# Optimization experiments

Hardware: AMD Instinct MI355X
Metric: run time of the kernel (lower is better)

The kernel has to match this reference:

```python
import jax, jax.numpy as jnp
import numpy as np

B, T, Fd, C, D = 16, 256, 128, 32, 32
K_RATIO = 0.5
EPS = 1e-5


def setup_inputs() -> dict:
    key = jax.random.key(0)
    ks = jax.random.split(key, 40)
    n = lambda i, shape, s=0.05: jax.random.normal(ks[i], shape, jnp.float32) * s
    inp = {"x": jax.random.normal(ks[0], (B, T, Fd, C), jnp.float32)}
    inp.update(c1w=n(1, (C, C)), c1b=n(2, (C,)), bng=1.0 + n(3, (C,)), bnb=n(4, (C,)),
               bnm=n(5, (C,)), bnv=jax.random.uniform(ks[6], (C,)) + 0.5,
               c2w=n(7, (1, C)), c2b=n(8, (1,)))
    def gat_params(i0, pre):
        return {pre + "apw": n(i0, (D, C)), pre + "apb": n(i0 + 1, (D,)),
                pre + "aw": n(i0 + 2, (D,)), pre + "pww": n(i0 + 3, (D, C)),
                pre + "pwb": n(i0 + 4, (D,)), pre + "pow": n(i0 + 5, (D, C)),
                pre + "pob": n(i0 + 6, (D,)), pre + "g": 1.0 + n(i0 + 7, (D,)),
                pre + "be": n(i0 + 8, (D,)), pre + "m": n(i0 + 9, (D,)),
                pre + "v": jax.random.uniform(ks[i0 + 10], (D,)) + 0.5}
    inp.update(gat_params(9, "fc_"))
    inp.update(gat_params(20, "tc_"))
    inp.update(pfw=n(31, (1, D)), pfb=n(32, (1,)), ptw=n(33, (1, D)), ptb=n(34, (1,)),
               w1=n(35, (D, D)), w2=n(36, (D, D)), fcw=n(37, (2, 2 * D)), fcb=n(38, (2,)))
    return inp


def _gat(h, apw, apb, aw, pww, pwb, poww, pob, g, be, mu, var):
    # h: (B, N, C). Dense pairwise multiplication -> (B, N, N, C)
    p = h[:, :, None, :] * h[:, None, :, :]
    e = jnp.tanh(jnp.einsum('bijc,dc->bijd', p, apw) + apb)      # (B,N,N,D)
    att = jax.nn.softmax(jnp.einsum('bijd,d->bij', e, aw), axis=2)  # softmax over dim=-2 (temp=1)
    out = jnp.einsum('bij,bjc->bic', att, h) @ pww.T + pwb + h @ poww.T + pob
    out = (out - mu) / jnp.sqrt(var + EPS) * g + be               # BatchNorm1d (eval)
    return jax.nn.selu(out)


def _pool(h, pw, pb, ratio):
    s = jax.nn.sigmoid(h @ pw.T + pb)                # (B,N,1)
    kn = max(int(h.shape[1] * ratio), 1)
    _, idx = jax.lax.top_k(s[..., 0], kn)            # (B,kn), descending scores
    return jnp.take_along_axis(h * s, idx[..., None], axis=1)


def reference(x, c1w, c1b, bng, bnb, bnm, bnv, c2w, c2b,
              fc_apw, fc_apb, fc_aw, fc_pww, fc_pwb, fc_pow, fc_pob, fc_g, fc_be, fc_m, fc_v,
              tc_apw, tc_apb, tc_aw, tc_pww, tc_pwb, tc_pow, tc_pob, tc_g, tc_be, tc_m, tc_v,
              pfw, pfb, ptw, ptb, w1, w2, fcw, fcb):
    # conv1 (1x1), SELU, BatchNorm2d (eval), conv2 (1x1 -> 1 channel)
    xp = jnp.einsum('oc,btfc->botf', c1w, x) + c1b[None, :, None, None]
    xp = jax.nn.selu(xp)
    xp = (xp - bnm[None, :, None, None]) / jnp.sqrt(bnv + EPS)[None, :, None, None] \
         * bng[None, :, None, None] + bnb[None, :, None, None]
    m = jnp.einsum('c,bctf->btf', c2w[0], xp) + c2b[0]           # (B,T,F)
    M0 = jax.nn.softmax(m, axis=1)
    FCatt = jnp.einsum('btf,btfc->bfc', M0, x)                   # sum over T
    TCatt = jnp.einsum('btf,btfc->btc', M0, x)                   # sum over F
    FC_gat = _gat(FCatt, fc_apw, fc_apb, fc_aw, fc_pww, fc_pwb, fc_pow, fc_pob, fc_g, fc_be, fc_m, fc_v)
    TC_gat = _gat(TCatt, tc_apw, tc_apb, tc_aw, tc_pww, tc_pwb, tc_pow, tc_pob, tc_g, tc_be, tc_m, tc_v)
    xF = _pool(FC_gat, pfw, pfb, K_RATIO)                        # (B, F/2, D)
    xT = _pool(TC_gat, ptw, ptb, K_RATIO)                        # (B, T/2, D)
    M1 = jax.nn.softmax((xF @ w1.T) @ xT.transpose(0, 2, 1), axis=-1)
    M2 = jax.nn.softmax((xT @ w2.T) @ xF.transpose(0, 2, 1), axis=-1)
    xF_fused = xF + M1 @ xT
    xT_fused = xT + M2 @ xF
    node = jnp.concatenate([xF_fused.max(axis=1), xT_fused.max(axis=1)], axis=-1)
    return node @ fcw.T + fcb
```

## Files before the change

kernel.cpp:

```cpp
#include <hip/hip_runtime.h>
#include <hip/hip_bf16.h>

#define Bn 16
#define Tn 256
#define Fn 128
#define Cn 32
#define Dn 32
#define EPSf 1e-5f
#define SELU_L 1.0507009873554805f
#define SELU_A 1.6732632423543772f

typedef unsigned short u16;
typedef unsigned int u32;
typedef __attribute__((ext_vector_type(8))) short bf16x8;
typedef __attribute__((ext_vector_type(4))) float f32x4;

struct Ptrs { const void* p[39]; };

#define P_C1W 0
#define P_C1B 1024
#define P_MW  1056
#define P_MK  1088
#define P_FC  1089
#define P_TCG (1089+3264)
#define G_APW 0
#define G_APB 1024
#define G_AW  1056
#define G_PWW 1088
#define G_PWB 2112
#define G_POW 2144
#define G_POB 3168
#define G_GS  3200
#define G_GB  3232
#define GAT_SZ 3264
#define P_PFW (P_TCG+GAT_SZ)
#define P_PFB (P_PFW+32)
#define P_PTW (P_PFB+1)
#define P_PTB (P_PTW+32)
#define P_W1  (P_PTB+1)
#define P_W2  (P_W1+1024)
#define P_FCW (P_W2+1024)
#define P_FCB (P_FCW+128)
#define P_FLAG 10000

#define WS_M     10240
#define WS_FCATT (WS_M+524288)
#define WS_TCATT (WS_FCATT+65536)
#define WS_FCGAT (WS_TCATT+131072)
#define WS_TCGAT (WS_FCGAT+65536)
#define WS_XF    (WS_TCGAT+131072)
#define WS_XT    (WS_XF+32768)
#define WS_XFF   (WS_XT+65536)
#define WS_XTF   (WS_XFF+32768)

__device__ __forceinline__ float bf2f(u16 u) {
    union { u32 i; float f; } v; v.i = ((u32)u) << 16; return v.f;
}
__device__ __forceinline__ u16 f2bf(float f) {
    union { float f; u32 u; } v; v.f = f;
    u32 r = (v.u + 0x7fffu + ((v.u >> 16) & 1u)) >> 16;
    return (u16)r;
}
__device__ __forceinline__ u32 cvt_pk_bf16(float lo, float hi) {
    u32 r;
    asm("v_cvt_pk_bf16_f32 %0, %1, %2" : "=v"(r) : "v"(lo), "v"(hi));
    return r;
}
__device__ __forceinline__ void up2(u32 u, float* o) {
    union { u32 i; float f; } a, b;
    a.i = u << 16; b.i = u & 0xffff0000u;
    o[0] = a.f; o[1] = b.f;
}
__device__ __forceinline__ float tanh_fast(float x) {
    float e = __expf(2.f * x);
    return 1.f - 2.f / (e + 1.f);
}
__device__ __forceinline__ float ldp(const void* p, int i, int isb) {
    return isb ? bf2f(((const u16*)p)[i]) : ((const float*)p)[i];
}

__global__ __launch_bounds__(256) void k0_setup(Ptrs in, float* __restrict__ P) {
    __shared__ int sflag;
    int tid = threadIdx.x;
    int blk = blockIdx.x;
    if (tid < 64) {
        const u16* xu = (const u16*)in.p[0];
        int bad = 0;
        #pragma unroll
        for (int q = 0; q < 4; q++) {
            float f = bf2f(xu[tid * 4 + q]);
            float a = fabsf(f);
            if (!(a < 64.f) && !(a == 0.f)) bad++;
        }
        #pragma unroll
        for (int off = 32; off >= 1; off >>= 1) bad += __shfl_xor(bad, off, 64);
        if (tid == 0) sflag = (bad <= 8) ? 1 : 0;
    }
    __syncthreads();
    const int isb = sflag;

    if (blk == 0) {
        if (tid == 0) P[P_FLAG] = (float)isb;
        for (int i = tid; i < 1024; i += 256) P[P_C1W + i] = ldp(in.p[1], i, isb);
        if (tid < 32) {
            float A = ldp(in.p[3], tid, isb) * rsqrtf(ldp(in.p[6], tid, isb) + EPSf);
            float w = ldp(in.p[7], tid, isb);
            P[P_C1B + tid] = ldp(in.p[2], tid, isb);
            P[P_MW + tid] = w * A * SELU_L;
            float Bc = ldp(in.p[4], tid, isb) - ldp(in.p[5], tid, isb) * A;
            float term = w * Bc;
            #pragma unroll
            for (int off = 16; off >= 1; off >>= 1) term += __shfl_xor(term, off, 64);
            if (tid == 0) P[P_MK] = term + ldp(in.p[8], 0, isb);
        }
        if (tid >= 64 && tid < 96) {
            int t = tid - 64;
            P[P_PFW + t] = ldp(in.p[31], t, isb);
            P[P_PTW + t] = ldp(in.p[33], t, isb);
        }
        if (tid == 96) { P[P_PFB] = ldp(in.p[32], 0, isb); P[P_PTB] = ldp(in.p[34], 0, isb); }
        if (tid == 97) P[P_FCB]     = ldp(in.p[38], 0, isb);
        if (tid == 98) P[P_FCB + 1] = ldp(in.p[38], 1, isb);
        if (tid >= 128) P[P_FCW + (tid - 128)] = ldp(in.p[37], tid - 128, isb);
    } else if (blk <= 2) {
        int g = blk - 1;
        int ib = g ? 20 : 9;
        float* G = P + (g ? P_TCG : P_FC);
        for (int i = tid; i < 1024; i += 256) {
            G[G_APW + i] = ldp(in.p[ib + 0], i, isb);
            G[G_PWW + i] = ldp(in.p[ib + 3], i, isb);
            G[G_POW + i] = ldp(in.p[ib + 5], i, isb);
        }
        if (tid < 32) {
            G[G_APB + tid] = ldp(in.p[ib + 1], tid, isb);
            G[G_AW  + tid] = ldp(in.p[ib + 2], tid, isb);
            G[G_PWB + tid] = ldp(in.p[ib + 4], tid, isb);
            G[G_POB + tid] = ldp(in.p[ib + 6], tid, isb);
            float gs = ldp(in.p[ib + 7], tid, isb) * rsqrtf(ldp(in.p[ib + 10], tid, isb) + EPSf);
            G[G_GS + tid] = gs;
            G[G_GB + tid] = ldp(in.p[ib + 8], tid, isb) - ldp(in.p[ib + 9], tid, isb) * gs;
        }
    } else {
        for (int i = tid; i < 1024; i += 256) {
            P[P_W1 + i] = ldp(in.p[35], i, isb);
            P[P_W2 + i] = ldp(in.p[36], i, isb);
        }
    }
}

__global__ __launch_bounds__(256) void k1_conv_m(const void* __restrict__ xin,
                                                 const float* __restrict__ P,
                                                 float* __restrict__ M) {
    const int isb = __builtin_amdgcn_readfirstlane((int)P[P_FLAG]);
    int tid = threadIdx.x;
    if (isb) {
        int w = tid >> 6, lane = tid & 63;
        int n = lane & 15, g = lane >> 4, kc = g * 8;
        union { u32 u[4]; bf16x8 v; } B0, B1;
        #pragma unroll
        for (int e = 0; e < 4; e++) {
            B0.u[e] = cvt_pk_bf16(P[P_C1W + n * 32 + kc + 2 * e],
                                  P[P_C1W + n * 32 + kc + 2 * e + 1]);
            B1.u[e] = cvt_pk_bf16(P[P_C1W + (n + 16) * 32 + kc + 2 * e],
                                  P[P_C1W + (n + 16) * 32 + kc + 2 * e + 1]);
        }
        float cb0v[4], cb1v[4], mw0v[4], mw1v[4];
        #pragma unroll
        for (int r = 0; r < 4; r++) {
            cb0v[r] = P[P_C1B + g * 4 + r];
            cb1v[r] = P[P_C1B + 16 + g * 4 + r];
            mw0v[r] = P[P_MW + g * 4 + r];
            mw1v[r] = P[P_MW + 16 + g * 4 + r];
        }
        float mk = P[P_MK];
        int rowblk = blockIdx.x * 256 + w * 64;
        const u16* xp = (const u16*)xin + (size_t)rowblk * 32;
        bf16x8 a[4];
        #pragma unroll
        for (int s = 0; s < 4; s++)
            a[s] = *(const bf16x8*)(xp + ((size_t)s * 16 + n) * 32 + kc);
        #pragma unroll
        for (int s = 0; s < 4; s++) {
            f32x4 c0 = {0.f, 0.f, 0.f, 0.f}, c1 = {0.f, 0.f, 0.f, 0.f};
            c0 = __builtin_amdgcn_mfma_f32_16x16x32_bf16(B0.v, a[s], c0, 0, 0, 0);
            c1 = __builtin_amdgcn_mfma_f32_16x16x32_bf16(B1.v, a[s], c1, 0, 0, 0);
            float part = 0.f;
            #pragma unroll
            for (int r = 0; r < 4; r++) {
                float z0 = c0[r] + cb0v[r], z1 = c1[r] + cb1v[r];
                float s0 = (z0 > 0.f) ? z0 : SELU_A * (__expf(z0) - 1.f);
                float s1 = (z1 > 0.f) ? z1 : SELU_A * (__expf(z1) - 1.f);
                part = fmaf(mw0v[r], s0, part);
                part = fmaf(mw1v[r], s1, part);
            }
            part += __shfl_xor(part, 16, 64);
            part += __shfl_xor(part, 32, 64);
            if (lane < 16) M[(size_t)rowblk + s * 16 + n] = part + mk;
        }
    } else {
        int idx = blockIdx.x * 256 + tid;
        float xv[32];
        const float4* xf4 = reinterpret_cast<const float4*>((const float*)xin + (size_t)idx * 32);
        #pragma unroll
        for (int q = 0; q < 8; q++) {
            float4 v = xf4[q];
            xv[q * 4 + 0] = v.x; xv[q * 4 + 1] = v.y;
            xv[q * 4 + 2] = v.z; xv[q * 4 + 3] = v.w;
        }
        float acc = P[P_MK];
        #pragma unroll
        for (int o = 0; o < 32; o++) {
            float z = P[P_C1B + o];
            #pragma unroll
            for (int c = 0; c < 32; c++) z = fmaf(P[P_C1W + o * 32 + c], xv[c], z);
            float br = (z > 0.f) ? z : SELU_A * (__expf(z) - 1.f);
            acc = fmaf(P[P_MW + o], br, acc);
        }
        M[idx] = acc;
    }
}

__global__ __launch_bounds__(256) void k2_softmax(float* __restrict__ M,
                                                  float* __restrict__ FCzero) {
    __shared__ float wred[4][16];
    int b = blockIdx.x >> 3, fg = blockIdx.x & 7;
    int tid = threadIdx.x;
    int w = tid >> 6, lane = tid & 63;
    int fq = tid & 3, tt = tid >> 2;
    float* colb = M + (size_t)b * (Tn * Fn) + fg * 16 + fq * 4;
    float4 v[4];
    float mx[4] = {-1e30f, -1e30f, -1e30f, -1e30f};
    #pragma unroll
    for (int p = 0; p < 4; p++) {
        v[p] = *(float4*)(colb + (size_t)(tt + p * 64) * Fn);
        mx[0] = fmaxf(mx[0], v[p].x); mx[1] = fmaxf(mx[1], v[p].y);
        mx[2] = fmaxf(mx[2], v[p].z); mx[3] = fmaxf(mx[3], v[p].w);
    }
    #pragma unroll
    for (int off = 4; off <= 32; off <<= 1) {
        #pragma unroll
        for (int c = 0; c < 4; c++) mx[c] = fmaxf(mx[c], __shfl_xor(mx[c], off, 64));
    }
    if (lane < 4) {
        #pragma unroll
        for (int c = 0; c < 4; c++) wred[w][lane * 4 + c] = mx[c];
    }
    __syncthreads();
    #pragma unroll
    for (int c = 0; c < 4; c++)
        mx[c] = fmaxf(fmaxf(wred[0][fq * 4 + c], wred[1][fq * 4 + c]),
                      fmaxf(wred[2][fq * 4 + c], wred[3][fq * 4 + c]));
    float4 e[4];
    float sm[4] = {0.f, 0.f, 0.f, 0.f};
    #pragma unroll
    for (int p = 0; p < 4; p++) {
        e[p].x = __expf(v[p].x - mx[0]); sm[0] += e[p].x;
        e[p].y = __expf(v[p].y - mx[1]); sm[1] += e[p].y;
        e[p].z = __expf(v[p].z - mx[2]); sm[2] += e[p].z;
        e[p].w = __expf(v[p].w - mx[3]); sm[3] += e[p].w;
    }
    #pragma unroll
    for (int off = 4; off <= 32; off <<= 1) {
        #pragma unroll
        for (int c = 0; c < 4; c++) sm[c] += __shfl_xor(sm[c], off, 64);
    }
    __syncthreads();
    if (lane < 4) {
        #pragma unroll
        for (int c = 0; c < 4; c++) wred[w][lane * 4 + c] = sm[c];
    }
    __syncthreads();
    float inv[4];
    #pragma unroll
    for (int c = 0; c < 4; c++)
        inv[c] = 1.f / (wred[0][fq * 4 + c] + wred[1][fq * 4 + c] +
                        wred[2][fq * 4 + c] + wred[3][fq * 4 + c]);
    #pragma unroll
    for (int p = 0; p < 4; p++) {
        float4 o4 = make_float4(e[p].x * inv[0], e[p].y * inv[1],
                                e[p].z * inv[2], e[p].w * inv[3]);
        *(float4*)(colb + (size_t)(tt + p * 64) * Fn) = o4;
    }
    int gid = blockIdx.x * 256 + tid;
    for (int i = gid; i < Bn * Fn * Cn; i += 128 * 256) FCzero[i] = 0.f;
}

__global__ __launch_bounds__(256) void k3n(const void* __restrict__ xin,
                                           const float* __restrict__ M,
                                           const float* __restrict__ Pflag,
                                           float* __restrict__ FCatt,
                                           float* __restrict__ TCatt) {
    __shared__ float part[4][8][32];
    int bi = blockIdx.x;
    int b = bi >> 5, tg = bi & 31;
    int tid = threadIdx.x;
    int w = tid >> 6, lane = tid & 63;
    const int isb = __builtin_amdgcn_readfirstlane((int)Pflag[P_FLAG]);
    float fa0[8], fa1[8];
    #pragma unroll
    for (int k = 0; k < 8; k++) { fa0[k] = 0.f; fa1[k] = 0.f; }
    int fbase = tid >> 4;
    for (int tt = 0; tt < 8; tt++) {
        int t = tg * 8 + tt;
        const float* Mrow = M + (size_t)b * (Tn * Fn) + (size_t)t * Fn;
        size_t rowoff = ((size_t)b * Tn + t) * (Fn * Cn);
        float ts0 = 0.f, ts1 = 0.f;
        #pragma unroll
        for (int k = 0; k < 8; k++) {
            float x0, x1;
            if (isb) {
                u32 u = *(const u32*)((const u16*)xin + rowoff + tid * 2 + 512 * k);
                float tmp[2]; up2(u, tmp); x0 = tmp[0]; x1 = tmp[1];
            } else {
                float2 v2 = *(const float2*)((const float*)xin + rowoff + tid * 2 + 512 * k);
                x0 = v2.x; x1 = v2.y;
            }
            float m = Mrow[fbase + 16 * k];
            x0 *= m; x1 *= m;
            fa0[k] += x0; fa1[k] += x1;
            ts0 += x0; ts1 += x1;
        }
        ts0 += __shfl_xor(ts0, 16, 64); ts0 += __shfl_xor(ts0, 32, 64);
        ts1 += __shfl_xor(ts1, 16, 64); ts1 += __shfl_xor(ts1, 32, 64);
        if (lane < 16) {
            part[w][tt][lane * 2]     = ts0;
            part[w][tt][lane * 2 + 1] = ts1;
        }
    }
    __syncthreads();
    {
        int tt = tid >> 5, c = tid & 31;
        float s = part[0][tt][c] + part[1][tt][c] + part[2][tt][c] + part[3][tt][c];
        TCatt[((size_t)b * Tn + tg * 8 + tt) * Cn + c] = s;
    }
    #pragma unroll
    for (int k = 0; k < 8; k++) {
        atomicAdd(&FCatt[(size_t)b * 4096 + tid * 2 + 512 * k],     fa0[k]);
        atomicAdd(&FCatt[(size_t)b * 4096 + tid * 2 + 512 * k + 1], fa1[k]);
    }
}

template<int NT>
__device__ __forceinline__ void gat_row(const float* __restrict__ h,
                                        const float* __restrict__ G,
                                        float* __restrict__ out,
                                        int i, int lane) {
    int n = lane & 15, g = lane >> 4, kc = g * 8;
    union { u32 u[4]; bf16x8 v; } B0, B1;
    #pragma unroll
    for (int e = 0; e < 4; e++) {
        B0.u[e] = cvt_pk_bf16(G[G_APW + n * 32 + kc + 2 * e],
                              G[G_APW + n * 32 + kc + 2 * e + 1]);
        B1.u[e] = cvt_pk_bf16(G[G_APW + (n + 16) * 32 + kc + 2 * e],
                              G[G_APW + (n + 16) * 32 + kc + 2 * e + 1]);
    }
    float awv0[4], awv1[4], abv0[4], abv1[4];
    #pragma unroll
    for (int r = 0; r < 4; r++) {
        awv0[r] = G[G_AW + g * 4 + r];
        awv1[r] = G[G_AW + 16 + g * 4 + r];
        abv0[r] = G[G_APB + g * 4 + r];
        abv1[r] = G[G_APB + 16 + g * 4 + r];
    }
    float hi[8];
    {
        const float4* hip = (const float4*)(h + (size_t)i * 32 + kc);
        float4 v0 = hip[0], v1 = hip[1];
        hi[0] = v0.x; hi[1] = v0.y; hi[2] = v0.z; hi[3] = v0.w;
        hi[4] = v1.x; hi[5] = v1.y; hi[6] = v1.z; hi[7] = v1.w;
    }
    float sc[NT];
    #pragma unroll
    for (int jt = 0; jt < NT; jt++) {
        const float4* hjp = (const float4*)(h + ((size_t)jt * 16 + n) * 32 + kc);
        float4 v0 = hjp[0], v1 = hjp[1];
        union { u32 u[4]; bf16x8 v; } A;
        A.u[0] = cvt_pk_bf16(hi[0] * v0.x, hi[1] * v0.y);
        A.u[1] = cvt_pk_bf16(hi[2] * v0.z, hi[3] * v0.w);
        A.u[2] = cvt_pk_bf16(hi[4] * v1.x, hi[5] * v1.y);
        A.u[3] = cvt_pk_bf16(hi[6] * v1.z, hi[7] * v1.w);
        f32x4 c0 = {0.f, 0.f, 0.f, 0.f}, c1 = {0.f, 0.f, 0.f, 0.f};
        c0 = __builtin_amdgcn_mfma_f32_16x16x32_bf16(B0.v, A.v, c0, 0, 0, 0);
        c1 = __builtin_amdgcn_mfma_f32_16x16x32_bf16(B1.v, A.v, c1, 0, 0, 0);
        float part = 0.f;
        #pragma unroll
        for (int r = 0; r < 4; r++) {
            part = fmaf(awv0[r], tanh_fast(c0[r] + abv0[r]), part);
            part = fmaf(awv1[r], tanh_fast(c1[r] + abv1[r]), part);
        }
        part += __shfl_xor(part, 16, 64);
        part += __shfl_xor(part, 32, 64);
        sc[jt] = part;
    }
    float mx = -1e30f;
    #pragma unroll
    for (int jt = 0; jt < NT; jt++) mx = fmaxf(mx, sc[jt]);
    #pragma unroll
    for (int off = 1; off < 16; off <<= 1) mx = fmaxf(mx, __shfl_xor(mx, off, 64));
    float sum = 0.f;
    #pragma unroll
    for (int jt = 0; jt < NT; jt++) { sc[jt] = __expf(sc[jt] - mx); sum += sc[jt]; }
    #pragma unroll
    for (int off = 1; off < 16; off <<= 1) sum += __shfl_xor(sum, off, 64);
    float inv = 1.f / sum;
    float attp[8] = {0.f, 0.f, 0.f, 0.f, 0.f, 0.f, 0.f, 0.f};
    #pragma unroll
    for (int jt = 0; jt < NT; jt++) {
        const float4* hjp = (const float4*)(h + ((size_t)jt * 16 + n) * 32 + kc);
        float4 v0 = hjp[0], v1 = hjp[1];
        float p = sc[jt];
        attp[0] = fmaf(p, v0.x, attp[0]); attp[1] = fmaf(p, v0.y, attp[1]);
        attp[2] = fmaf(p, v0.z, attp[2]); attp[3] = fmaf(p, v0.w, attp[3]);
        attp[4] = fmaf(p, v1.x, attp[4]); attp[5] = fmaf(p, v1.y, attp[5]);
        attp[6] = fmaf(p, v1.z, attp[6]); attp[7] = fmaf(p, v1.w, attp[7]);
    }
    #pragma unroll
    for (int off = 1; off < 16; off <<= 1) {
        #pragma unroll
        for (int e = 0; e < 8; e++) attp[e] += __shfl_xor(attp[e], off, 64);
    }
    #pragma unroll
    for (int e = 0; e < 8; e++) attp[e] *= inv;
    float att[32], hif[32];
    #pragma unroll
    for (int gg = 0; gg < 4; gg++) {
        #pragma unroll
        for (int e = 0; e < 8; e++) {
            att[gg * 8 + e] = __shfl(attp[e], gg << 4, 64);
            hif[gg * 8 + e] = __shfl(hi[e],  gg << 4, 64);
        }
    }
    int d = lane & 31;
    float z = G[G_PWB + d] + G[G_POB + d];
    #pragma unroll
    for (int c = 0; c < 32; c++)
        z = fmaf(G[G_PWW + d * 32 + c], att[c], fmaf(G[G_POW + d * 32 + c], hif[c], z));
    z = z * G[G_GS + d] + G[G_GB + d];
    z = SELU_L * ((z > 0.f) ? z : SELU_A * (__expf(z) - 1.f));
    if (lane < 32) out[(size_t)i * 32 + d] = z;
}

__global__ __launch_bounds__(256) void k4ab(const float* __restrict__ P,
                                            const float* __restrict__ FCatt,
                                            const float* __restrict__ TCatt,
                                            float* __restrict__ FCgat,
                                            float* __restrict__ TCgat) {
    int bi = blockIdx.x, tid = threadIdx.x;
    int w = tid >> 6, lane = tid & 63;
    if (bi < 512) {
        int b = bi >> 5, i = (bi & 31) * 4 + w;
        gat_row<8>(FCatt + (size_t)b * 4096, P + P_FC, FCgat + (size_t)b * 4096, i, lane);
    } else {
        int u = bi - 512;
        int b = u >> 6, i = (u & 63) * 4 + w;
        gat_row<16>(TCatt + (size_t)b * 8192, P + P_TCG, TCgat + (size_t)b * 8192, i, lane);
    }
}

__global__ __launch_bounds__(256) void k5_pool(const float* __restrict__ P,
                                               const float* __restrict__ FCgat,
                                               const float* __restrict__ TCgat,
                                               float* __restrict__ XF,
                                               float* __restrict__ XT) {
    __shared__ float s[256];
    int bi = blockIdx.x;
    int N, kn, b, pboff; const float* g; float* xp; const float* pw;
    if (bi < 16) { b = bi; N = 128; kn = 64;
        g = FCgat + (size_t)b * 4096; xp = XF + (size_t)b * 2048; pw = P + P_PFW; pboff = P_PFB; }
    else { b = bi - 16; N = 256; kn = 128;
        g = TCgat + (size_t)b * 8192; xp = XT + (size_t)b * 4096; pw = P + P_PTW; pboff = P_PTB; }
    int tid = threadIdx.x;
    float sv = 0.f;
    if (tid < N) {
        float z = P[pboff];
        #pragma unroll
        for (int d = 0; d < 32; d++) z = fmaf(pw[d], g[(size_t)tid * 32 + d], z);
        sv = 1.f / (1.f + __expf(-z));
        s[tid] = sv;
    }
    __syncthreads();
    if (tid < N) {
        int rank = 0;
        for (int l = 0; l < N; l++) {
            float sl = s[l];
            rank += (sl > sv) || (sl == sv && l < tid);
        }
        if (rank < kn) {
            #pragma unroll
            for (int d = 0; d < 32; d++) xp[(size_t)rank * 32 + d] = g[(size_t)tid * 32 + d] * sv;
        }
    }
}

__global__ __launch_bounds__(256) void k6_fuse(const float* __restrict__ P,
                                               const float* __restrict__ XF,
                                               const float* __restrict__ XT,
                                               float* __restrict__ XFF,
                                               float* __restrict__ XTF) {
    int wid = blockIdx.x * 4 + (threadIdx.x >> 6);
    int lane = threadIdx.x & 63;
    if (wid < 1024) {
        int b = wid >> 6, i = wid & 63;
        const float* xf  = XF + ((size_t)b * 64 + i) * 32;
        const float* xtb = XT + (size_t)b * 4096;
        const float* w1 = P + P_W1;
        int d = lane & 31;
        float y = 0.f;
        #pragma unroll
        for (int c = 0; c < 32; c++) y = fmaf(w1[d * 32 + c], xf[c], y);
        float xtr0[32], xtr1[32];
        #pragma unroll
        for (int c = 0; c < 32; c++) {
            xtr0[c] = xtb[(size_t)lane * 32 + c];
            xtr1[c] = xtb[(size_t)(lane + 64) * 32 + c];
        }
        float s0 = 0.f, s1 = 0.f;
        #pragma unroll
        for (int c = 0; c < 32; c++) {
            float yc = __shfl(y, c, 64);
            s0 = fmaf(yc, xtr0[c], s0);
            s1 = fmaf(yc, xtr1[c], s1);
        }
        float mx = fmaxf(s0, s1);
        #pragma unroll
        for (int off = 1; off < 64; off <<= 1) mx = fmaxf(mx, __shfl_xor(mx, off, 64));
        float e0 = __expf(s0 - mx), e1 = __expf(s1 - mx);
        float sm = e0 + e1;
        #pragma unroll
        for (int off = 1; off < 64; off <<= 1) sm += __shfl_xor(sm, off, 64);
        float inv = 1.f / sm;
        float a0 = e0 * inv, a1 = e1 * inv;
        float v[32];
        #pragma unroll
        for (int c = 0; c < 32; c++) v[c] = a0 * xtr0[c] + a1 * xtr1[c];
        #pragma unroll
        for (int off = 1; off < 64; off <<= 1) {
            #pragma unroll
            for (int c = 0; c < 32; c++) v[c] += __shfl_xor(v[c], off, 64);
        }
        if (lane == 0) {
            float* o = XFF + ((size_t)b * 64 + i) * 32;
            #pragma unroll
            for (int c = 0; c < 32; c++) o[c] = xf[c] + v[c];
        }
    } else {
        int r = wid - 1024;
        int b = r >> 7, i = r & 127;
        const float* xt  = XT + ((size_t)b * 128 + i) * 32;
        const float* xfb = XF + (size_t)b * 2048;
        const float* w2 = P + P_W2;
        int d = lane & 31;
        float y = 0.f;
        #pragma unroll
        for (int c = 0; c < 32; c++) y = fmaf(w2[d * 32 + c], xt[c], y);
        float xfr[32];
        #pragma unroll
        for (int c = 0; c < 32; c++) xfr[c] = xfb[(size_t)lane * 32 + c];
        float sc0 = 0.f;
        #pragma unroll
        for (int c = 0; c < 32; c++) sc0 = fmaf(__shfl(y, c, 64), xfr[c], sc0);
        float mx = sc0;
        #pragma unroll
        for (int off = 1; off < 64; off <<= 1) mx = fmaxf(mx, __shfl_xor(mx, off, 64));
        float e = __expf(sc0 - mx);
        float sm = e;
        #pragma unroll
        for (int off = 1; off < 64; off <<= 1) sm += __shfl_xor(sm, off, 64);
        float a = e / sm;
        float v[32];
        #pragma unroll
        for (int c = 0; c < 32; c++) v[c] = a * xfr[c];
        #pragma unroll
        for (int off = 1; off < 64; off <<= 1) {
            #pragma unroll
            for (int c = 0; c < 32; c++) v[c] += __shfl_xor(v[c], off, 64);
        }
        if (lane == 0) {
            float* o = XTF + ((size_t)b * 128 + i) * 32;
            #pragma unroll
            for (int c = 0; c < 32; c++) o[c] = xt[c] + v[c];
        }
    }
}

__global__ __launch_bounds__(64) void k7_out(const float* __restrict__ P,
                                             const float* __restrict__ XFF,
                                             const float* __restrict__ XTF,
                                             void* __restrict__ outp) {
    __shared__ float node[64];
    int b = blockIdx.x, tid = threadIdx.x;
    if (tid < 32) {
        float m = -1e30f;
        for (int r = 0; r < 64; r++) m = fmaxf(m, XFF[((size_t)b * 64 + r) * 32 + tid]);
        node[tid] = m;
    } else {
        int c = tid - 32;
        float m = -1e30f;
        for (int r = 0; r < 128; r++) m = fmaxf(m, XTF[((size_t)b * 128 + r) * 32 + c]);
        node[tid] = m;
    }
    __syncthreads();
    if (tid < 2) {
        float z = P[P_FCB + tid];
        #pragma unroll
        for (int k = 0; k < 64; k++) z = fmaf(P[P_FCW + tid * 64 + k], node[k], z);
        int isb = (int)P[P_FLAG];
        if (isb) ((u16*)outp)[b * 2 + tid] = f2bf(z);
        else     ((float*)outp)[b * 2 + tid] = z;
    }
}

extern "C" void kernel_launch(void* const* d_in, const int* in_sizes, int n_in,
                              void* d_out, int out_size, void* d_ws, size_t ws_size,
                              hipStream_t stream) {
    (void)in_sizes; (void)n_in; (void)out_size; (void)ws_size;
    float* W = (float*)d_ws;
    Ptrs ptrs;
    for (int i = 0; i < 39; i++) ptrs.p[i] = d_in[i];
    const void* x = d_in[0];
    float* P = W;

    k0_setup<<<4, 256, 0, stream>>>(ptrs, P);
    k1_conv_m<<<2048, 256, 0, stream>>>(x, P, W + WS_M);
    k2_softmax<<<128, 256, 0, stream>>>(W + WS_M, W + WS_FCATT);
    k3n<<<512, 256, 0, stream>>>(x, W + WS_M, P, W + WS_FCATT, W + WS_TCATT);
    k4ab<<<1536, 256, 0, stream>>>(P, W + WS_FCATT, W + WS_TCATT,
                                   W + WS_FCGAT, W + WS_TCGAT);
    k5_pool<<<32, 256, 0, stream>>>(P, W + WS_FCGAT, W + WS_TCGAT, W + WS_XF, W + WS_XT);
    k6_fuse<<<768, 256, 0, stream>>>(P, W + WS_XF, W + WS_XT, W + WS_XFF, W + WS_XTF);
    k7_out<<<16, 64, 0, stream>>>(P, W + WS_XFF, W + WS_XTF, d_out);
}
```

Before: 319.8 us.

## Split TC GAT rows across two waves with LDS softmax merge

The TC-graph GAT path now gives each output row two wavefronts, each covering half of the j columns with its own partial max, sum and weighted accumulation. The two halves are merged in shared memory using a log-sum-exp style rescale, and the first wave computes the projection, BN and SELU. This shortens the serial per-row chain and doubles the TC block count to raise parallelism and latency hiding. The cost is an added block barrier, LDS traffic, and the second wave sitting idle during the epilogue.

```diff
diff --git a/kernel.cpp b/kernel.cpp
--- a/kernel.cpp
+++ b/kernel.cpp
@@ -450,10 +450,122 @@
     if (bi < 512) {
         int b = bi >> 5, i = (bi & 31) * 4 + w;
         gat_row<8>(FCatt + (size_t)b * 4096, P + P_FC, FCgat + (size_t)b * 4096, i, lane);
-    } else {
-        int u = bi - 512;
-        int b = u >> 6, i = (u & 63) * 4 + w;
-        gat_row<16>(TCatt + (size_t)b * 8192, P + P_TCG, TCgat + (size_t)b * 8192, i, lane);
+        return;
+    }
+    __shared__ float lds[4][36];
+    int u = bi - 512;
+    int b = u >> 7;
+    int rp = u & 127;
+    int i = rp * 2 + (w >> 1);
+    int hf = w & 1;
+    const float* h = TCatt + (size_t)b * 8192;
+    const float* G = P + P_TCG;
+    float* out = TCgat + (size_t)b * 8192;
+    int n = lane & 15, g = lane >> 4, kc = g * 8;
+
+    union { u32 u4[4]; bf16x8 v; } B0, B1;
+    #pragma unroll
+    for (int e = 0; e < 4; e++) {
+        B0.u4[e] = cvt_pk_bf16(G[G_APW + n * 32 + kc + 2 * e],
+                               G[G_APW + n * 32 + kc + 2 * e + 1]);
+        B1.u4[e] = cvt_pk_bf16(G[G_APW + (n + 16) * 32 + kc + 2 * e],
+                               G[G_APW + (n + 16) * 32 + kc + 2 * e + 1]);
+    }
+    float awv0[4], awv1[4], abv0[4], abv1[4];
+    #pragma unroll
+    for (int r = 0; r < 4; r++) {
+        awv0[r] = G[G_AW + g * 4 + r];
+        awv1[r] = G[G_AW + 16 + g * 4 + r];
+        abv0[r] = G[G_APB + g * 4 + r];
+        abv1[r] = G[G_APB + 16 + g * 4 + r];
+    }
+    float hi[8];
+    {
+        const float4* hip = (const float4*)(h + (size_t)i * 32 + kc);
+        float4 v0 = hip[0], v1 = hip[1];
+        hi[0] = v0.x; hi[1] = v0.y; hi[2] = v0.z; hi[3] = v0.w;
+        hi[4] = v1.x; hi[5] = v1.y; hi[6] = v1.z; hi[7] = v1.w;
+    }
+    float sc[8];
+    #pragma unroll
+    for (int q = 0; q < 8; q++) {
+        int jt = hf * 8 + q;
+        const float4* hjp = (const float4*)(h + ((size_t)jt * 16 + n) * 32 + kc);
+        float4 v0 = hjp[0], v1 = hjp[1];
+        union { u32 u4[4]; bf16x8 v; } A;
+        A.u4[0] = cvt_pk_bf16(hi[0] * v0.x, hi[1] * v0.y);
+        A.u4[1] = cvt_pk_bf16(hi[2] * v0.z, hi[3] * v0.w);
+        A.u4[2] = cvt_pk_bf16(hi[4] * v1.x, hi[5] * v1.y);
+        A.u4[3] = cvt_pk_bf16(hi[6] * v1.z, hi[7] * v1.w);
+        f32x4 c0 = {0.f, 0.f, 0.f, 0.f}, c1 = {0.f, 0.f, 0.f, 0.f};
+        c0 = __builtin_amdgcn_mfma_f32_16x16x32_bf16(B0.v, A.v, c0, 0, 0, 0);
+        c1 = __builtin_amdgcn_mfma_f32_16x16x32_bf16(B1.v, A.v, c1, 0, 0, 0);
+        float part = 0.f;
+        #pragma unroll
+        for (int r = 0; r < 4; r++) {
+            part = fmaf(awv0[r], tanh_fast(c0[r] + abv0[r]), part);
+            part = fmaf(awv1[r], tanh_fast(c1[r] + abv1[r]), part);
+        }
+        part += __shfl_xor(part, 16, 64);
+        part += __shfl_xor(part, 32, 64);
+        sc[q] = part;
+    }
+    float mh = -1e30f;
+    #pragma unroll
+    for (int q = 0; q < 8; q++) mh = fmaxf(mh, sc[q]);
+    #pragma unroll
+    for (int off = 1; off < 16; off <<= 1) mh = fmaxf(mh, __shfl_xor(mh, off, 64));
+    float sh = 0.f;
+    #pragma unroll
+    for (int q = 0; q < 8; q++) { sc[q] = __expf(sc[q] - mh); sh += sc[q]; }
+    #pragma unroll
+    for (int off = 1; off < 16; off <<= 1) sh += __shfl_xor(sh, off, 64);
+    float attp[8] = {0.f, 0.f, 0.f, 0.f, 0.f, 0.f, 0.f, 0.f};
+    #pragma unroll
+    for (int q = 0; q < 8; q++) {
+        int jt = hf * 8 + q;
+        const float4* hjp = (const float4*)(h + ((size_t)jt * 16 + n) * 32 + kc);
+        float4 v0 = hjp[0], v1 = hjp[1];
+        float p = sc[q];
+        attp[0] = fmaf(p, v0.x, attp[0]); attp[1] = fmaf(p, v0.y, attp[1]);
+        attp[2] = fmaf(p, v0.z, attp[2]); attp[3] = fmaf(p, v0.w, attp[3]);
+        attp[4] = fmaf(p, v1.x, attp[4]); attp[5] = fmaf(p, v1.y, attp[5]);
+        attp[6] = fmaf(p, v1.z, attp[6]); attp[7] = fmaf(p, v1.w, attp[7]);
+    }
+    #pragma unroll
+    for (int off = 1; off < 16; off <<= 1) {
+        #pragma unroll
+        for (int e = 0; e < 8; e++) attp[e] += __shfl_xor(attp[e], off, 64);
+    }
+    if (n == 0) {
+        #pragma unroll
+        for (int e = 0; e < 8; e++) lds[w][2 + g * 8 + e] = attp[e];
+    }
+    if (lane == 0) { lds[w][0] = mh; lds[w][1] = sh; }
+    __syncthreads();
+    if (hf == 0) {
+        int wp = w + 1;
+        float m0 = lds[w][0],  s0 = lds[w][1];
+        float m1 = lds[wp][0], s1 = lds[wp][1];
+        float Mx = fmaxf(m0, m1);
+        float e0 = __expf(m0 - Mx), e1 = __expf(m1 - Mx);
+        float inv = 1.f / (s0 * e0 + s1 * e1);
+        float hif[32];
+        #pragma unroll
+        for (int gg = 0; gg < 4; gg++) {
+            #pragma unroll
+            for (int e = 0; e < 8; e++) hif[gg * 8 + e] = __shfl(hi[e], gg << 4, 64);
+        }
+        int d = lane & 31;
+        float z = G[G_PWB + d] + G[G_POB + d];
+        #pragma unroll
+        for (int c = 0; c < 32; c++) {
+            float att = (lds[w][2 + c] * e0 + lds[wp][2 + c] * e1) * inv;
+            z = fmaf(G[G_PWW + d * 32 + c], att, fmaf(G[G_POW + d * 32 + c], hif[c], z));
+        }
+        z = z * G[G_GS + d] + G[G_GB + d];
+        z = SELU_L * ((z > 0.f) ? z : SELU_A * (__expf(z) - 1.f));
+        if (lane < 32) out[(size_t)i * 32 + d] = z;
     }
 }
 
@@ -624,7 +736,7 @@
     k1_conv_m<<<2048, 256, 0, stream>>>(x, P, W + WS_M);
     k2_softmax<<<128, 256, 0, stream>>>(W + WS_M, W + WS_FCATT);
     k3n<<<512, 256, 0, stream>>>(x, W + WS_M, P, W + WS_FCATT, W + WS_TCATT);
-    k4ab<<<1536, 256, 0, stream>>>(P, W + WS_FCATT, W + WS_TCATT,
+    k4ab<<<2560, 256, 0, stream>>>(P, W + WS_FCATT, W + WS_TCATT,
                                    W + WS_FCGAT, W + WS_TCGAT);
     k5_pool<<<32, 256, 0, stream>>>(P, W + WS_FCGAT, W + WS_TCGAT, W + WS_XF, W + WS_XT);
     k6_fuse<<<768, 256, 0, stream>>>(P, W + WS_XF, W + WS_XT, W + WS_XFF, W + WS_XTF);
```

New measurement: 311.7 us. -2.5%, faster.
